# Optimization experiments

Hardware: AMD Instinct MI355X
Metric: run time of the kernel (lower is better)

Reference implementation:

```python
import jax, jax.numpy as jnp
import numpy as np

K = 3  # kernel size


def _qparams(t):
    # dynamic per-tensor affine quant params: scale=(max-min)/255, zero=-round(min/scale)
    mx = jnp.max(t)
    mn = jnp.min(t)
    s = (mx - mn) / 255.0
    z = -jnp.round(mn / s)
    return s, z


def _quant(t, s, z):
    return jnp.clip(jnp.round(t / s + z), 0.0, 255.0).astype(jnp.int32)


def setup_inputs() -> dict:
    key = jax.random.key(0)
    k1, k2, k3 = jax.random.split(key, 3)
    x = jax.random.normal(k1, (4, 32, 34, 34), dtype=jnp.float32)
    weight = jax.random.normal(k2, (64, 32, K, K), dtype=jnp.float32) * 0.1
    bias = jax.random.normal(k3, (64,), dtype=jnp.float32) * 0.1
    a = jnp.arange(256, dtype=jnp.float32)
    lut = a[:, None] * a[None, :]
    return {"x": x, "weight": weight, "lut": lut, "bias": bias}


def reference(x, weight, lut, bias):
    OC = weight.shape[0]
    # --- dynamic per-tensor quantization of activations and weights ---
    s_x, z_x = _qparams(x)
    s_w, z_w = _qparams(weight)
    qx = _quant(x, s_x, z_x)                       # [B, C, H, W] uint8 codes (int32)
    qw = _quant(weight, s_w, z_w).reshape(OC, -1)  # [OC, C*K*K]

    # --- im2col on the quantized activations (VALID, stride 1) ---
    patches = jax.lax.conv_general_dilated_patches(
        qx.astype(jnp.float32), (K, K), (1, 1), 'VALID')  # [B, C*K*K, OH, OW]
    B, CKK, OH, OW = patches.shape
    qxp = patches.astype(jnp.int32).transpose(0, 2, 3, 1).reshape(B, OH * OW, CKK)

    # --- LUT-based approximate multiply-accumulate ---
    # idx[b, p, oc, k] = qxp[b, p, k] * 256 + qw[oc, k]
    idx = qxp[:, :, None, :] * 256 + qw[None, None, :, :]          # [B, P, OC, CKK]
    acc = jnp.take(lut.reshape(-1), idx).sum(axis=-1)              # [B, P, OC]

    # --- affine dequantization of the integer accumulator ---
    sum_qw = qw.sum(axis=-1).astype(jnp.float32)                   # [OC]
    sum_qx = qxp.sum(axis=-1).astype(jnp.float32)                  # [B, P]
    out = s_x * s_w * (acc
                       - z_x * sum_qw[None, None, :]
                       - z_w * sum_qx[:, :, None]
                       + CKK * z_x * z_w)                          # [B, P, OC]
    out = out.reshape(B, OH, OW, OC).transpose(0, 3, 1, 2)         # [B, OC, OH, OW]
    return out + bias[None, :, None, None]
```

## Files before the change

### kernel.cpp

```cpp
#include <hip/hip_runtime.h>
#include <stdint.h>

#define B_    4
#define C_    32
#define HW_   34
#define OC_   64
#define CKK_  288

#define NX (B_*C_*HW_*HW_)
#define NW (OC_*C_*9)
#define NX4 (NX/4)
#define NW4 (NW/4)

__device__ __forceinline__ unsigned dot4(unsigned a, unsigned b, unsigned acc) {
#if __has_builtin(__builtin_amdgcn_udot4)
  return __builtin_amdgcn_udot4(a, b, acc, false);
#else
  acc += (a & 0xFFu) * (b & 0xFFu);
  acc += ((a >> 8) & 0xFFu) * ((b >> 8) & 0xFFu);
  acc += ((a >> 16) & 0xFFu) * ((b >> 16) & 0xFFu);
  acc += (a >> 24) * (b >> 24);
  return acc;
#endif
}

__device__ __forceinline__ void red4(float4 v, float& mx, float& mn) {
  mx = fmaxf(mx, fmaxf(fmaxf(v.x, v.y), fmaxf(v.z, v.w)));
  mn = fminf(mn, fminf(fminf(v.x, v.y), fminf(v.z, v.w)));
}

__global__ __launch_bounds__(256) void fused_kernel(const float* __restrict__ x,
                                                    const float* __restrict__ w,
                                                    const float* __restrict__ bias,
                                                    float* __restrict__ out) {
  const int och = blockIdx.x;
  const int oh  = blockIdx.y;
  const int b   = blockIdx.z;
  const int t   = threadIdx.x;

  __shared__ unsigned s_qw[32 * 32 * 4];
  __shared__ unsigned s_pt[32 * 32 * 4];
  __shared__ int s_sumqw[32];
  __shared__ float s_red[4][4];
  __shared__ float s_par[4];

  for (int i = t; i < 32 * 32 * 4; i += 256) { s_qw[i] = 0; s_pt[i] = 0; }

  float xmx = -3.402823466e38f, xmn = 3.402823466e38f;
  float wmx = -3.402823466e38f, wmn = 3.402823466e38f;
  {
    const float4* x4 = (const float4*)x;
    #pragma unroll 1
    for (int base = 0; base < 144 * 256; base += 16 * 256) {
      float4 v[16];
      #pragma unroll
      for (int k = 0; k < 16; k++) v[k] = x4[base + (k << 8) + t];
      #pragma unroll
      for (int k = 0; k < 16; k++) red4(v[k], xmx, xmn);
    }
    if (t < 128) {
      float4 v = x4[144 * 256 + t];
      red4(v, xmx, xmn);
    }
  }
  {
    const float4* w4 = (const float4*)w;
    float4 v[18];
    #pragma unroll
    for (int k = 0; k < 18; k++) v[k] = w4[(k << 8) + t];
    #pragma unroll
    for (int k = 0; k < 18; k++) red4(v[k], wmx, wmn);
  }
  for (int m = 32; m; m >>= 1) {
    xmx = fmaxf(xmx, __shfl_xor(xmx, m, 64));
    xmn = fminf(xmn, __shfl_xor(xmn, m, 64));
    wmx = fmaxf(wmx, __shfl_xor(wmx, m, 64));
    wmn = fminf(wmn, __shfl_xor(wmn, m, 64));
  }
  const int wid = t >> 6, lane = t & 63;
  if (lane == 0) {
    s_red[wid][0] = xmx; s_red[wid][1] = xmn;
    s_red[wid][2] = wmx; s_red[wid][3] = wmn;
  }
  __syncthreads();
  if (t == 0) {
    float mxx = fmaxf(fmaxf(s_red[0][0], s_red[1][0]), fmaxf(s_red[2][0], s_red[3][0]));
    float mnx = fminf(fminf(s_red[0][1], s_red[1][1]), fminf(s_red[2][1], s_red[3][1]));
    float mxw = fmaxf(fmaxf(s_red[0][2], s_red[1][2]), fmaxf(s_red[2][2], s_red[3][2]));
    float mnw = fminf(fminf(s_red[0][3], s_red[1][3]), fminf(s_red[2][3], s_red[3][3]));
    float sx = (mxx - mnx) / 255.0f;
    float sw = (mxw - mnw) / 255.0f;
    s_par[0] = sx;
    s_par[1] = -rintf(mnx / sx);
    s_par[2] = sw;
    s_par[3] = -rintf(mnw / sw);
  }
  __syncthreads();
  const float s_x = s_par[0], z_x = s_par[1], s_w = s_par[2], z_w = s_par[3];

  {
    const float* wsrc = w + och * (32 * CKK_);
    unsigned char* qb = (unsigned char*)s_qw;
    #pragma unroll
    for (int i = 0; i < 36; i++) {
      int idx = t + i * 256;
      float v = wsrc[idx] / s_w + z_w;
      int q = (int)rintf(v);
      q = min(max(q, 0), 255);
      int ocl = idx / CKK_;
      int k   = idx - ocl * CKK_;
      int c   = k / 9;
      int kr  = k - c * 9;
      int r   = kr / 3;
      int kw  = kr - r * 3;
      qb[(ocl * 32 + (c ^ ((ocl >> 1) & 7))) * 16 + r * 4 + kw] = (unsigned char)q;
    }
  }
  {
    const float* xsrc = x + (size_t)b * (C_ * HW_ * HW_);
    unsigned char* pb = (unsigned char*)s_pt;
    #pragma unroll
    for (int i = 0; i < 13; i++) {
      int idx = t + i * 256;
      if (idx < 32 * 3 * HW_) {
        int c   = idx / (3 * HW_);
        int rem = idx - c * (3 * HW_);
        int r   = rem / HW_;
        int wc  = rem - r * HW_;
        float v = xsrc[(c * HW_ + (oh + r)) * HW_ + wc] / s_x + z_x;
        int q = (int)rintf(v);
        q = min(max(q, 0), 255);
        #pragma unroll
        for (int kw = 0; kw < 3; kw++) {
          int ow = wc - kw;
          if (0 <= ow && ow < 32)
            pb[(ow * 32 + (c ^ ((ow >> 1) & 7))) * 16 + r * 4 + kw] = (unsigned char)q;
        }
      }
    }
  }
  __syncthreads();

  if (t < 32) {
    unsigned s = 0;
    const unsigned* row = s_qw + t * 128;
    for (int i = 0; i < 128; i++) s = dot4(row[i], 0x01010101u, s);
    s_sumqw[t] = (int)s;
  }

  const int owp = t & 15, ocp = t >> 4;
  const int ow0 = owp * 2, oc0 = ocp * 2;
  const unsigned psw = (unsigned)(owp & 7);
  const unsigned wsw = (unsigned)(ocp & 7);

  unsigned a00 = 0, a01 = 0, a10 = 0, a11 = 0, sx0 = 0, sx1 = 0;
  const uint4* qw4 = (const uint4*)s_qw;
  const uint4* pt4 = (const uint4*)s_pt;
  #pragma unroll 8
  for (int c = 0; c < 32; c++) {
    uint4 w0 = qw4[oc0 * 32 + (c ^ wsw)];
    uint4 w1 = qw4[(oc0 + 1) * 32 + (c ^ wsw)];
    uint4 p0 = pt4[ow0 * 32 + (c ^ psw)];
    uint4 p1 = pt4[(ow0 + 1) * 32 + (c ^ psw)];
    a00 = dot4(p0.x, w0.x, a00); a00 = dot4(p0.y, w0.y, a00); a00 = dot4(p0.z, w0.z, a00);
    a01 = dot4(p0.x, w1.x, a01); a01 = dot4(p0.y, w1.y, a01); a01 = dot4(p0.z, w1.z, a01);
    a10 = dot4(p1.x, w0.x, a10); a10 = dot4(p1.y, w0.y, a10); a10 = dot4(p1.z, w0.z, a10);
    a11 = dot4(p1.x, w1.x, a11); a11 = dot4(p1.y, w1.y, a11); a11 = dot4(p1.z, w1.z, a11);
    sx0 = dot4(p0.x, 0x01010101u, sx0); sx0 = dot4(p0.y, 0x01010101u, sx0); sx0 = dot4(p0.z, 0x01010101u, sx0);
    sx1 = dot4(p1.x, 0x01010101u, sx1); sx1 = dot4(p1.y, 0x01010101u, sx1); sx1 = dot4(p1.z, 0x01010101u, sx1);
  }
  __syncthreads();

  const float sxw = s_x * s_w;
  const float zz  = 288.0f * z_x * z_w;
  const int ocg0 = och * 32 + oc0;
  const float bz0 = bias[ocg0], bz1 = bias[ocg0 + 1];
  const float sqw0 = (float)s_sumqw[oc0], sqw1 = (float)s_sumqw[oc0 + 1];
  const float fs0 = (float)(int)sx0, fs1 = (float)(int)sx1;

  float2 r0, r1;
  r0.x = sxw * ((float)(int)a00 - z_x * sqw0 - z_w * fs0 + zz) + bz0;
  r0.y = sxw * ((float)(int)a10 - z_x * sqw0 - z_w * fs1 + zz) + bz0;
  r1.x = sxw * ((float)(int)a01 - z_x * sqw1 - z_w * fs0 + zz) + bz1;
  r1.y = sxw * ((float)(int)a11 - z_x * sqw1 - z_w * fs1 + zz) + bz1;

  float* obase = out + ((((size_t)b * OC_ + ocg0) * 32 + oh) * 32 + ow0);
  *(float2*)obase = r0;
  *(float2*)(obase + 32 * 32) = r1;
}

extern "C" void kernel_launch(void* const* d_in, const int* in_sizes, int n_in,
                              void* d_out, int out_size, void* d_ws, size_t ws_size,
                              hipStream_t stream) {
  const float* x    = (const float*)d_in[0];
  const float* w    = (const float*)d_in[1];
  const float* bias = (const float*)d_in[3];

  dim3 grid(2, 32, 4);
  fused_kernel<<<grid, 256, 0, stream>>>(x, w, bias, (float*)d_out);
}
```

Baseline: 78.86 us.

## Double-buffer min/max loads, stagger per-block start offsets, prefetch quant inputs early

The global min/max reduction over x now uses two register buffers so the next batch of loads is in flight while the current batch is reduced. Each block starts its sweep at a different rotated offset to spread L2/HBM traffic across channels instead of all 256 blocks hitting the same lines together. The weight and activation values needed for quantization are loaded into registers before the parameter barrier, so their latency overlaps the reduction. This raises register pressure considerably (launch bounds set to one block per CU), which could spill or reduce occupancy.

```diff
diff --git a/kernel.cpp b/kernel.cpp
--- a/kernel.cpp
+++ b/kernel.cpp
@@ -7,10 +7,6 @@
 #define OC_   64
 #define CKK_  288
 
-#define NX (B_*C_*HW_*HW_)
-#define NW (OC_*C_*9)
-#define NX4 (NX/4)
-#define NW4 (NW/4)
 
 __device__ __forceinline__ unsigned dot4(unsigned a, unsigned b, unsigned acc) {
 #if __has_builtin(__builtin_amdgcn_udot4)
@@ -29,14 +25,15 @@
   mn = fminf(mn, fminf(fminf(v.x, v.y), fminf(v.z, v.w)));
 }
 
-__global__ __launch_bounds__(256) void fused_kernel(const float* __restrict__ x,
-                                                    const float* __restrict__ w,
-                                                    const float* __restrict__ bias,
-                                                    float* __restrict__ out) {
+__global__ __launch_bounds__(256, 1) void fused_kernel(const float* __restrict__ x,
+                                                       const float* __restrict__ w,
+                                                       const float* __restrict__ bias,
+                                                       float* __restrict__ out) {
   const int och = blockIdx.x;
   const int oh  = blockIdx.y;
   const int b   = blockIdx.z;
   const int t   = threadIdx.x;
+  const int bid = (blockIdx.z * 32 + blockIdx.y) * 2 + blockIdx.x;
 
   __shared__ unsigned s_qw[32 * 32 * 4];
   __shared__ unsigned s_pt[32 * 32 * 4];
@@ -48,29 +45,64 @@
 
   float xmx = -3.402823466e38f, xmn = 3.402823466e38f;
   float wmx = -3.402823466e38f, wmn = 3.402823466e38f;
-  {
-    const float4* x4 = (const float4*)x;
-    #pragma unroll 1
-    for (int base = 0; base < 144 * 256; base += 16 * 256) {
-      float4 v[16];
-      #pragma unroll
-      for (int k = 0; k < 16; k++) v[k] = x4[base + (k << 8) + t];
-      #pragma unroll
-      for (int k = 0; k < 16; k++) red4(v[k], xmx, xmn);
+
+  const float4* x4 = (const float4*)x;
+  const float4* w4 = (const float4*)w;
+  const int rot = (bid * 5) % 144;
+
+  float4 va[16], vb[16], vtail;
+  const bool has_tail = (t < 128);
+
+#define XSLOT(S) (((S) >= 144 ? (S) - 144 : (S)))
+#define LOADX(dst, sbatch) { _Pragma("unroll") \
+    for (int k = 0; k < 16; k++) { int s_ = rot + (sbatch) * 16 + k; \
+      dst[k] = x4[(XSLOT(s_) << 8) + t]; } }
+#define REDX(src) { _Pragma("unroll") \
+    for (int k = 0; k < 16; k++) red4(src[k], xmx, xmn); }
+
+  if (has_tail) vtail = x4[144 * 256 + t];
+  LOADX(va, 0);
+  #pragma unroll 1
+  for (int sb = 0; sb < 8; sb += 2) {
+    LOADX(vb, sb + 1);
+    REDX(va);
+    LOADX(va, sb + 2);
+    REDX(vb);
+  }
+
+  const int wrot = bid % 18;
+  float4 wv[18];
+  #pragma unroll
+  for (int k = 0; k < 18; k++) {
+    int s_ = wrot + k; if (s_ >= 18) s_ -= 18;
+    wv[k] = w4[(s_ << 8) + t];
+  }
+
+  REDX(va);
+  if (has_tail) red4(vtail, xmx, xmn);
+
+  const float* wsrc = w + och * (32 * CKK_);
+  float wq[36];
+  #pragma unroll
+  for (int i = 0; i < 36; i++) wq[i] = wsrc[t + i * 256];
+
+  const float* xsrc = x + (size_t)b * (C_ * HW_ * HW_);
+  float xq[13];
+  #pragma unroll
+  for (int i = 0; i < 13; i++) {
+    int idx = t + i * 256;
+    if (idx < 32 * 3 * HW_) {
+      int c   = idx / (3 * HW_);
+      int rem = idx - c * (3 * HW_);
+      int r   = rem / HW_;
+      int wc  = rem - r * HW_;
+      xq[i] = xsrc[(c * HW_ + (oh + r)) * HW_ + wc];
     }
-    if (t < 128) {
-      float4 v = x4[144 * 256 + t];
-      red4(v, xmx, xmn);
-    }
-  }
-  {
-    const float4* w4 = (const float4*)w;
-    float4 v[18];
-    #pragma unroll
-    for (int k = 0; k < 18; k++) v[k] = w4[(k << 8) + t];
-    #pragma unroll
-    for (int k = 0; k < 18; k++) red4(v[k], wmx, wmn);
-  }
+  }
+
+  #pragma unroll
+  for (int k = 0; k < 18; k++) red4(wv[k], wmx, wmn);
+
   for (int m = 32; m; m >>= 1) {
     xmx = fmaxf(xmx, __shfl_xor(xmx, m, 64));
     xmn = fminf(xmn, __shfl_xor(xmn, m, 64));
@@ -99,12 +131,11 @@
   const float s_x = s_par[0], z_x = s_par[1], s_w = s_par[2], z_w = s_par[3];
 
   {
-    const float* wsrc = w + och * (32 * CKK_);
     unsigned char* qb = (unsigned char*)s_qw;
     #pragma unroll
     for (int i = 0; i < 36; i++) {
       int idx = t + i * 256;
-      float v = wsrc[idx] / s_w + z_w;
+      float v = wq[i] / s_w + z_w;
       int q = (int)rintf(v);
       q = min(max(q, 0), 255);
       int ocl = idx / CKK_;
@@ -117,7 +148,6 @@
     }
   }
   {
-    const float* xsrc = x + (size_t)b * (C_ * HW_ * HW_);
     unsigned char* pb = (unsigned char*)s_pt;
     #pragma unroll
     for (int i = 0; i < 13; i++) {
@@ -127,7 +157,7 @@
         int rem = idx - c * (3 * HW_);
         int r   = rem / HW_;
         int wc  = rem - r * HW_;
-        float v = xsrc[(c * HW_ + (oh + r)) * HW_ + wc] / s_x + z_x;
+        float v = xq[i] / s_x + z_x;
         int q = (int)rintf(v);
         q = min(max(q, 0), 255);
         #pragma unroll
```

After: 75.55 us. 1.04x faster.
